# Optimization experiments

Hardware: AMD Instinct MI355X
Metric: run time of the kernel (lower is better)

The kernel has to match this reference:

```python
import jax, jax.numpy as jnp
import numpy as np

N, E, D, R, L = 30000, 200000, 768, 10, 2
EPS = 1e-5

def setup_inputs() -> dict:
    key = jax.random.key(0)
    ks = jax.random.split(key, 10)
    x = jax.random.normal(ks[0], (N, D), dtype=jnp.float32)
    edge_index = jax.random.randint(ks[1], (2, E), 0, N, dtype=jnp.int64)
    edge_type = jax.random.randint(ks[2], (E,), 0, R, dtype=jnp.int64)
    s = 0.02
    W_rel = jax.random.normal(ks[3], (L, R, D, D), dtype=jnp.float32) * s
    W_root = jax.random.normal(ks[4], (L, D, D), dtype=jnp.float32) * s
    bias = jax.random.normal(ks[5], (L, D), dtype=jnp.float32) * s
    ln_g = jnp.ones((L, D), dtype=jnp.float32)
    ln_b = jnp.zeros((L, D), dtype=jnp.float32)
    return {"x": x, "edge_index": edge_index, "edge_type": edge_type,
            "W_rel": W_rel, "W_root": W_root, "bias": bias,
            "ln_g": ln_g, "ln_b": ln_b}

def _layer_norm(h, g, b):
    mu = jnp.mean(h, axis=-1, keepdims=True)
    var = jnp.mean(jnp.square(h - mu), axis=-1, keepdims=True)
    return (h - mu) * jax.lax.rsqrt(var + EPS) * g + b

def _rgcn_conv(h, src, dst, etype, W_rel, W_root, b):
    # per-relation mean aggregation: segment id = dst * R + relation
    seg = dst * R + etype  # [E]
    msgs = h[src]  # [E, D] irregular gather
    sums = jax.ops.segment_sum(msgs, seg, num_segments=N * R)  # [N*R, D]
    cnts = jax.ops.segment_sum(jnp.ones((E,), h.dtype), seg, num_segments=N * R)
    means = sums / jnp.maximum(cnts, 1.0)[:, None]
    means = means.reshape(N, R, D)
    # linearity: mean_r(W_r x_j) == W_r mean_r(x_j)
    agg = jnp.einsum('nrd,rde->ne', means, W_rel)
    return agg + h @ W_root + b

def reference(x, edge_index, edge_type, W_rel, W_root, bias, ln_g, ln_b):
    src, dst = edge_index[0], edge_index[1]
    h = x
    for i in range(L):
        h_prev = h
        h = _rgcn_conv(h, src, dst, edge_type, W_rel[i], W_root[i], bias[i])
        h = _layer_norm(h, ln_g[i], ln_b[i])
        if i > 0:
            h = h + h_prev  # residual (skipped on first layer, per source)
        # dropout is identity in eval mode
        if i < L - 1:
            h = jax.nn.relu(h)
    return h
```

## Files before the change

### kernel.cpp

```cpp
#include <hip/hip_runtime.h>

#define N_NODES 30000
#define N_EDGES 200000
#define DIM 768
#define N_REL 10
#define N_LAYERS 2
#define LN_EPS 1e-5f
#define W_ELEMS (DIM * DIM)
#define BKS 64
#define GT_MAX 1573

typedef _Float16 f16;
typedef _Float16 f16x4 __attribute__((ext_vector_type(4)));
typedef _Float16 f16x8 __attribute__((ext_vector_type(8)));
typedef float f32x4 __attribute__((ext_vector_type(4)));

#define GLD(gaddr, laddr)                                                              \
    __builtin_amdgcn_global_load_lds((const __attribute__((address_space(1))) void*)(gaddr), \
                                     (__attribute__((address_space(3))) void*)(laddr), 16, 0, 0)

__global__ void count_kernel(const int* __restrict__ ei, const int* __restrict__ et,
                             int* __restrict__ cnt, int* __restrict__ deg,
                             int* __restrict__ posmap) {
    int e = blockIdx.x * blockDim.x + threadIdx.x;
    if (e >= N_EDGES) return;
    int src = ei[e];
    int dst = ei[N_EDGES + e];
    int r = et[e];
    atomicAdd(&cnt[dst * N_REL + r], 1);
    atomicAdd(&deg[dst], 1);
    posmap[r * N_NODES + src] = 1;
}

#define PSCAN_CHUNK 118
__global__ void posscan_kernel(int* __restrict__ posmap, int* __restrict__ mr) {
    __shared__ int part[256];
    const int r = blockIdx.x;
    int* pm = posmap + (size_t)r * N_NODES;
    const int t = threadIdx.x;
    const int c0 = t * PSCAN_CHUNK;
    int s = 0;
    for (int i = 0; i < PSCAN_CHUNK; ++i) {
        const int idx = c0 + i;
        if (idx < N_NODES && pm[idx] == 1) ++s;
    }
    part[t] = s;
    __syncthreads();
    if (t == 0) {
        int a = 0;
        for (int i = 0; i < 256; ++i) { const int v = part[i]; part[i] = a; a += v; }
        mr[r] = a;
    }
    __syncthreads();
    int a = part[t];
    for (int i = 0; i < PSCAN_CHUNK; ++i) {
        const int idx = c0 + i;
        if (idx < N_NODES && pm[idx] == 1) pm[idx] = a++;
    }
}

#define SCAN_CHUNK 118
__global__ void scan_kernel(const int* __restrict__ deg, int* __restrict__ row_start,
                            int* __restrict__ cursor) {
    __shared__ int part[256];
    __shared__ int off[257];
    const int t = threadIdx.x;
    const int c0 = t * SCAN_CHUNK;
    int s = 0;
    for (int i = 0; i < SCAN_CHUNK; ++i) {
        const int idx = c0 + i;
        if (idx < N_NODES) s += deg[idx];
    }
    part[t] = s;
    __syncthreads();
    if (t == 0) {
        int a = 0;
        for (int i = 0; i < 256; ++i) { off[i] = a; a += part[i]; }
        off[256] = a;
        row_start[N_NODES] = a;
    }
    __syncthreads();
    int a = off[t];
    for (int i = 0; i < SCAN_CHUNK; ++i) {
        const int idx = c0 + i;
        if (idx < N_NODES) {
            row_start[idx] = a;
            cursor[idx] = a;
            a += deg[idx];
        }
    }
}

__global__ void zprep_kernel(const int* __restrict__ mr, int* __restrict__ zbase,
                             int* __restrict__ tile_rel) {
    if (blockIdx.x == 0 && threadIdx.x == 0) {
        int zc = 0, tc = 0;
        for (int r = 0; r < N_REL; ++r) {
            zbase[r] = zc;
            const int nt = (mr[r] + 127) >> 7;
            for (int i = 0; i < nt; ++i) tile_rel[tc + i] = r;
            tc += nt;
            zc += nt << 7;
        }
    }
}

__global__ void fill_kernel(const int* __restrict__ ei, const int* __restrict__ et,
                            const int* __restrict__ posmap, const int* __restrict__ zbase,
                            int* __restrict__ cursor, int* __restrict__ pack,
                            int* __restrict__ srclist) {
    int e = blockIdx.x * blockDim.x + threadIdx.x;
    if (e >= N_EDGES) return;
    int src = ei[e];
    int dst = ei[N_EDGES + e];
    int r = et[e];
    const int zrow = zbase[r] + posmap[r * N_NODES + src];
    int pos = atomicAdd(&cursor[dst], 1);
    pack[pos] = (r << 24) | zrow;
    srclist[zrow] = src;
}

__global__ void convx_kernel(const float* __restrict__ in, f16* __restrict__ out) {
    int idx = blockIdx.x * blockDim.x + threadIdx.x;
    if (idx >= N_NODES * DIM / 4) return;
    const float4 v = *reinterpret_cast<const float4*>(in + (size_t)idx * 4);
    f16x4 o = {(f16)v.x, (f16)v.y, (f16)v.z, (f16)v.w};
    *reinterpret_cast<f16x4*>(out + (size_t)idx * 4) = o;
}

__global__ void convw_kernel(const float* __restrict__ Wrel, const float* __restrict__ Wroot,
                             f16* __restrict__ WT, int layer) {
    __shared__ float tile[32][33];
    const int s = blockIdx.z;
    const float* src = (s < N_REL) ? (Wrel + ((size_t)layer * N_REL + s) * W_ELEMS)
                                   : (Wroot + (size_t)layer * W_ELEMS);
    const int k0 = blockIdx.x * 32;
    const int j0 = blockIdx.y * 32;
    const int tx = threadIdx.x;
    const int ty = threadIdx.y;
#pragma unroll
    for (int i = 0; i < 4; ++i)
        tile[ty + i * 8][tx] = src[(size_t)(k0 + ty + i * 8) * DIM + j0 + tx];
    __syncthreads();
    f16* dst = WT + (size_t)s * W_ELEMS;
#pragma unroll
    for (int i = 0; i < 4; ++i)
        dst[(size_t)(j0 + ty + i * 8) * DIM + k0 + tx] = (f16)tile[tx][ty + i * 8];
}

__global__ void __launch_bounds__(256)
gemm_kernel(const f16* __restrict__ A, const f16* __restrict__ WT,
            const int* __restrict__ srclist, const int* __restrict__ tile_rel,
            f16* __restrict__ Zout, float* __restrict__ aggout) {
    __shared__ alignas(128) f16 As[2][128 * BKS];
    __shared__ alignas(128) f16 Bs[2][128 * BKS];

    const int nwg = gridDim.x;
    const int orig = blockIdx.x;
    const int qq = nwg >> 3, rr = nwg & 7, xc = orig & 7, oo = orig >> 3;
    const int wg = (xc < rr ? xc * (qq + 1) : rr * (qq + 1) + (xc - rr) * qq) + oo;
    const int gt = wg / 6, jt = wg % 6;

    int rel;
    if (tile_rel != nullptr) {
        rel = tile_rel[gt];
        if (rel < 0) return;
    } else {
        rel = N_REL;
    }

    const int t = threadIdx.x;
    const int wv = t >> 6, lane = t & 63;
    const int wr = wv >> 1, wc = wv & 1;
    const f16* B = WT + (size_t)rel * W_ELEMS + (size_t)(jt * 128) * DIM;

    const f16* gA[4];
    const f16* gB[4];
#pragma unroll
    for (int q = 0; q < 4; ++q) {
        const int chunk = q * 256 + t;
        const int row = chunk >> 3;
        const int gk = (chunk & 7) ^ (row & 7);
        int arow;
        if (tile_rel != nullptr) {
            arow = srclist[gt * 128 + row];
        } else {
            arow = gt * 128 + row;
            if (arow > N_NODES - 1) arow = N_NODES - 1;
        }
        gA[q] = A + (size_t)arow * DIM + gk * 8;
        gB[q] = B + (size_t)row * DIM + gk * 8;
    }

    f32x4 acc[4][4];
#pragma unroll
    for (int i = 0; i < 4; ++i)
#pragma unroll
        for (int j = 0; j < 4; ++j) acc[i][j] = (f32x4){0.f, 0.f, 0.f, 0.f};

    const int lr16 = lane & 15, lk = lane >> 4, l7 = lane & 7;

#pragma unroll
    for (int q = 0; q < 4; ++q) {
        GLD(gA[q], (char*)As[0] + q * 4096 + wv * 1024);
        GLD(gB[q], (char*)Bs[0] + q * 4096 + wv * 1024);
    }
    __syncthreads();

    for (int ks = 0; ks < DIM / BKS; ++ks) {
        const int cur = ks & 1;
        if (ks < DIM / BKS - 1) {
#pragma unroll
            for (int q = 0; q < 4; ++q) {
                GLD(gA[q] + (ks + 1) * BKS, (char*)As[cur ^ 1] + q * 4096 + wv * 1024);
                GLD(gB[q] + (ks + 1) * BKS, (char*)Bs[cur ^ 1] + q * 4096 + wv * 1024);
            }
        }
#pragma unroll
        for (int h = 0; h < 2; ++h) {
            f16x8 a[4], b[4];
            const int cp = (((h << 2) | lk) ^ l7) * 8;
#pragma unroll
            for (int i = 0; i < 4; ++i) {
                a[i] = *(const f16x8*)&As[cur][(wr * 64 + i * 16 + lr16) * BKS + cp];
                b[i] = *(const f16x8*)&Bs[cur][(wc * 64 + i * 16 + lr16) * BKS + cp];
            }
#pragma unroll
            for (int mi = 0; mi < 4; ++mi)
#pragma unroll
                for (int ni = 0; ni < 4; ++ni)
                    acc[mi][ni] =
                        __builtin_amdgcn_mfma_f32_16x16x32_f16(a[mi], b[ni], acc[mi][ni], 0, 0, 0);
        }
        __syncthreads();
    }

    const int lrow = lk * 4, lcol = lr16;
    const int c0 = jt * 128 + wc * 64;
    if (tile_rel != nullptr) {
#pragma unroll
        for (int mi = 0; mi < 4; ++mi)
#pragma unroll
            for (int q = 0; q < 4; ++q) {
                const int z = gt * 128 + wr * 64 + mi * 16 + lrow + q;
                f16* zp = Zout + (size_t)z * DIM + c0 + lcol;
#pragma unroll
                for (int ni = 0; ni < 4; ++ni) zp[ni * 16] = (f16)acc[mi][ni][q];
            }
    } else {
#pragma unroll
        for (int mi = 0; mi < 4; ++mi)
#pragma unroll
            for (int q = 0; q < 4; ++q) {
                const int row = gt * 128 + wr * 64 + mi * 16 + lrow + q;
                if (row >= N_NODES) continue;
                float* op = aggout + (size_t)row * DIM + c0 + lcol;
#pragma unroll
                for (int ni = 0; ni < 4; ++ni) op[ni * 16] = acc[mi][ni][q];
            }
    }
}

__global__ void __launch_bounds__(192)
gather_kernel(const f16* __restrict__ Z, const int* __restrict__ row_start,
              const int* __restrict__ pack, const int* __restrict__ cnt,
              float* __restrict__ agg) {
    const int dst = blockIdx.x;
    const int lo = row_start[dst];
    const int hi = row_start[dst + 1];
    if (lo == hi) return;
    const int t = threadIdx.x;
    float a0 = 0.f, a1 = 0.f, a2 = 0.f, a3 = 0.f;
    for (int i = lo; i < hi; ++i) {
        const int p = pack[i];
        const int r = p >> 24;
        const int zrow = p & 0xFFFFFF;
        const float inv = 1.0f / (float)cnt[dst * N_REL + r];
        const f16x4 v = *reinterpret_cast<const f16x4*>(Z + (size_t)zrow * DIM + t * 4);
        a0 += (float)v[0] * inv;
        a1 += (float)v[1] * inv;
        a2 += (float)v[2] * inv;
        a3 += (float)v[3] * inv;
    }
    float* ap = agg + (size_t)dst * DIM + t * 4;
    float4 c = *reinterpret_cast<float4*>(ap);
    c.x += a0; c.y += a1; c.z += a2; c.w += a3;
    *reinterpret_cast<float4*>(ap) = c;
}

__device__ __forceinline__ float block_reduce_sum(float v, float* sm) {
#pragma unroll
    for (int o = 32; o > 0; o >>= 1) v += __shfl_down(v, o, 64);
    const int wid = threadIdx.x >> 6;
    const int lane = threadIdx.x & 63;
    __syncthreads();
    if (lane == 0) sm[wid] = v;
    __syncthreads();
    return sm[0] + sm[1] + sm[2] + sm[3];
}

__global__ void __launch_bounds__(256)
ln_kernel(const float* __restrict__ agg, const float* __restrict__ bias,
          const float* __restrict__ g, const float* __restrict__ beta,
          const f16* __restrict__ resid16, float* __restrict__ outf32,
          f16* __restrict__ outf16, int do_relu) {
    __shared__ float sm[4];
    const int n = blockIdx.x;
    const int t = threadIdx.x;
    float v[3];
    float s = 0.f;
#pragma unroll
    for (int i = 0; i < 3; ++i) {
        const int d = t + i * 256;
        v[i] = agg[(size_t)n * DIM + d] + bias[d];
        s += v[i];
    }
    const float mu = block_reduce_sum(s, sm) * (1.0f / DIM);
    float s2 = 0.f;
#pragma unroll
    for (int i = 0; i < 3; ++i) {
        const float c = v[i] - mu;
        s2 += c * c;
    }
    const float var = block_reduce_sum(s2, sm) * (1.0f / DIM);
    const float inv = rsqrtf(var + LN_EPS);
#pragma unroll
    for (int i = 0; i < 3; ++i) {
        const int d = t + i * 256;
        float o = (v[i] - mu) * inv * g[d] + beta[d];
        if (resid16 != nullptr) o += (float)resid16[(size_t)n * DIM + d];
        if (do_relu) o = fmaxf(o, 0.f);
        if (outf32 != nullptr) outf32[(size_t)n * DIM + d] = o;
        if (outf16 != nullptr) outf16[(size_t)n * DIM + d] = (f16)o;
    }
}

extern "C" void kernel_launch(void* const* d_in, const int* in_sizes, int n_in,
                              void* d_out, int out_size, void* d_ws, size_t ws_size,
                              hipStream_t stream) {
    const float* x      = (const float*)d_in[0];
    const int*   ei     = (const int*)d_in[1];
    const int*   et     = (const int*)d_in[2];
    const float* W_rel  = (const float*)d_in[3];
    const float* W_root = (const float*)d_in[4];
    const float* bias   = (const float*)d_in[5];
    const float* ln_g   = (const float*)d_in[6];
    const float* ln_b   = (const float*)d_in[7];
    float* out = (float*)d_out;

    char* w = (char*)d_ws;
    auto alloc = [&](size_t bytes) -> char* {
        char* p = w;
        w += (bytes + 255) & ~(size_t)255;
        return p;
    };
    f16* hf16      = (f16*)alloc((size_t)N_NODES * DIM * 2);
    f16* WT        = (f16*)alloc((size_t)(N_REL + 1) * W_ELEMS * 2);
    int* cnt       = (int*)alloc((size_t)N_NODES * N_REL * 4);
    int* deg       = (int*)alloc((size_t)N_NODES * 4);
    int* row_start = (int*)alloc((size_t)(N_NODES + 1) * 4);
    int* cursor    = (int*)alloc((size_t)N_NODES * 4);
    int* pack      = (int*)alloc((size_t)N_EDGES * 4);
    int* posmap    = (int*)alloc((size_t)N_REL * N_NODES * 4);
    int* mr        = (int*)alloc(64);
    int* zbase     = (int*)alloc(64);
    int* tile_rel  = (int*)alloc((size_t)GT_MAX * 4);
    int* srclist   = (int*)alloc((size_t)GT_MAX * 128 * 4);
    f16* Zg        = (f16*)w;

    hipMemsetAsync(cnt, 0, (size_t)N_NODES * N_REL * 4, stream);
    hipMemsetAsync(deg, 0, (size_t)N_NODES * 4, stream);
    hipMemsetAsync(posmap, 0xFF, (size_t)N_REL * N_NODES * 4, stream);
    hipMemsetAsync(tile_rel, 0xFF, (size_t)GT_MAX * 4, stream);
    hipMemsetAsync(srclist, 0, (size_t)GT_MAX * 128 * 4, stream);
    count_kernel<<<(N_EDGES + 255) / 256, 256, 0, stream>>>(ei, et, cnt, deg, posmap);
    posscan_kernel<<<N_REL, 256, 0, stream>>>(posmap, mr);
    scan_kernel<<<1, 256, 0, stream>>>(deg, row_start, cursor);
    zprep_kernel<<<1, 64, 0, stream>>>(mr, zbase, tile_rel);
    fill_kernel<<<(N_EDGES + 255) / 256, 256, 0, stream>>>(ei, et, posmap, zbase, cursor,
                                                           pack, srclist);
    convx_kernel<<<(N_NODES * DIM / 4 + 255) / 256, 256, 0, stream>>>(x, hf16);

    const int mt = (N_NODES + 127) / 128;
    for (int l = 0; l < N_LAYERS; ++l) {
        convw_kernel<<<dim3(24, 24, N_REL + 1), dim3(32, 8), 0, stream>>>(W_rel, W_root, WT, l);

        gemm_kernel<<<mt * 6, 256, 0, stream>>>(hf16, WT, nullptr, nullptr,
                                                (f16*)nullptr, out);
        gemm_kernel<<<GT_MAX * 6, 256, 0, stream>>>(hf16, WT, srclist, tile_rel, Zg, nullptr);
        gather_kernel<<<N_NODES, 192, 0, stream>>>(Zg, row_start, pack, cnt, out);

        ln_kernel<<<N_NODES, 256, 0, stream>>>(
            out, bias + (size_t)l * DIM, ln_g + (size_t)l * DIM, ln_b + (size_t)l * DIM,
            (l > 0) ? hf16 : nullptr,
            (l == N_LAYERS - 1) ? out : nullptr,
            (l < N_LAYERS - 1) ? hf16 : nullptr,
            (l < N_LAYERS - 1) ? 1 : 0);
    }
}
```

Before: 1.172 ms.

## Triple-buffer GEMM LDS tiles with one barrier per k-step

Moves the GEMM's shared-memory staging from double to triple buffering and issues loads two k-steps ahead. Explicit vmcnt waits and a single barrier per iteration replace the trailing __syncthreads. The aim is to hide more global-to-LDS latency and cut one barrier per step. It raises LDS use from 64KB to 96KB per block, which may lower occupancy, and it depends on getting the hand-written waitcnt accounting right.

```diff
diff --git a/kernel.cpp b/kernel.cpp
--- a/kernel.cpp
+++ b/kernel.cpp
@@ -8,6 +8,7 @@
 #define LN_EPS 1e-5f
 #define W_ELEMS (DIM * DIM)
 #define BKS 64
+#define NT (DIM / BKS)
 #define GT_MAX 1573
 
 typedef _Float16 f16;
@@ -152,8 +153,8 @@
 gemm_kernel(const f16* __restrict__ A, const f16* __restrict__ WT,
             const int* __restrict__ srclist, const int* __restrict__ tile_rel,
             f16* __restrict__ Zout, float* __restrict__ aggout) {
-    __shared__ alignas(128) f16 As[2][128 * BKS];
-    __shared__ alignas(128) f16 Bs[2][128 * BKS];
+    __shared__ alignas(128) f16 As[3][128 * BKS];
+    __shared__ alignas(128) f16 Bs[3][128 * BKS];
 
     const int nwg = gridDim.x;
     const int orig = blockIdx.x;
@@ -192,6 +193,14 @@
         gB[q] = B + (size_t)row * DIM + gk * 8;
     }
 
+#define STAGE(buf, ks)                                                                   \
+    do {                                                                                 \
+        _Pragma("unroll") for (int q = 0; q < 4; ++q) {                                  \
+            GLD(gA[q] + (ks) * BKS, (char*)As[buf] + q * 4096 + wv * 1024);              \
+            GLD(gB[q] + (ks) * BKS, (char*)Bs[buf] + q * 4096 + wv * 1024);              \
+        }                                                                                \
+    } while (0)
+
     f32x4 acc[4][4];
 #pragma unroll
     for (int i = 0; i < 4; ++i)
@@ -200,22 +209,21 @@
 
     const int lr16 = lane & 15, lk = lane >> 4, l7 = lane & 7;
 
-#pragma unroll
-    for (int q = 0; q < 4; ++q) {
-        GLD(gA[q], (char*)As[0] + q * 4096 + wv * 1024);
-        GLD(gB[q], (char*)Bs[0] + q * 4096 + wv * 1024);
-    }
-    __syncthreads();
-
-    for (int ks = 0; ks < DIM / BKS; ++ks) {
-        const int cur = ks & 1;
-        if (ks < DIM / BKS - 1) {
-#pragma unroll
-            for (int q = 0; q < 4; ++q) {
-                GLD(gA[q] + (ks + 1) * BKS, (char*)As[cur ^ 1] + q * 4096 + wv * 1024);
-                GLD(gB[q] + (ks + 1) * BKS, (char*)Bs[cur ^ 1] + q * 4096 + wv * 1024);
-            }
+    STAGE(0, 0);
+    STAGE(1, 1);
+
+#pragma unroll
+    for (int ks = 0; ks < NT; ++ks) {
+        const int cur = ks % 3;
+        if (ks == NT - 1) {
+            asm volatile("s_waitcnt vmcnt(0)" ::: "memory");
+        } else {
+            asm volatile("s_waitcnt vmcnt(8)" ::: "memory");
         }
+        __builtin_amdgcn_sched_barrier(0);
+        __builtin_amdgcn_s_barrier();
+        if (ks + 2 < NT) STAGE((ks + 2) % 3, ks + 2);
+
 #pragma unroll
         for (int h = 0; h < 2; ++h) {
             f16x8 a[4], b[4];
@@ -232,8 +240,8 @@
                     acc[mi][ni] =
                         __builtin_amdgcn_mfma_f32_16x16x32_f16(a[mi], b[ni], acc[mi][ni], 0, 0, 0);
         }
-        __syncthreads();
-    }
+    }
+#undef STAGE
 
     const int lrow = lk * 4, lcol = lr16;
     const int c0 = jt * 128 + wc * 64;
```

Result: slower. 1.350 ms (+15.2%).

## Merge root and relation GEMMs into one launch and fuse gather with layernorm

Applied to the files above, without the earlier changes.

The root-weight GEMM tiles are appended to the relation tile list, so a single GEMM launch covers both and the tail of one overlaps the other. The gather kernel now also applies bias, layer norm, residual and ReLU, using 4-wide vector accesses. This removes one launch and one read/write pass over the fp32 aggregate buffer per layer. Out-of-place gather writes back into the same out buffer per node row, so correctness relies on each block owning its own row.

```diff
diff --git a/kernel.cpp b/kernel.cpp
--- a/kernel.cpp
+++ b/kernel.cpp
@@ -8,7 +8,10 @@
 #define LN_EPS 1e-5f
 #define W_ELEMS (DIM * DIM)
 #define BKS 64
+#define NT (DIM / BKS)
 #define GT_MAX 1573
+#define N_ROOT_TILES ((N_NODES + 127) / 128)
+#define GT_ALL (GT_MAX + N_ROOT_TILES)
 
 typedef _Float16 f16;
 typedef _Float16 f16x4 __attribute__((ext_vector_type(4)));
@@ -102,6 +105,7 @@
             tc += nt;
             zc += nt << 7;
         }
+        for (int i = 0; i < N_ROOT_TILES; ++i) tile_rel[tc + i] = N_REL + i;
     }
 }
 
@@ -161,13 +165,10 @@
     const int wg = (xc < rr ? xc * (qq + 1) : rr * (qq + 1) + (xc - rr) * qq) + oo;
     const int gt = wg / 6, jt = wg % 6;
 
-    int rel;
-    if (tile_rel != nullptr) {
-        rel = tile_rel[gt];
-        if (rel < 0) return;
-    } else {
-        rel = N_REL;
-    }
+    const int v = tile_rel[gt];
+    if (v < 0) return;
+    const bool comp = (v < N_REL);
+    const int rel = comp ? v : N_REL;
 
     const int t = threadIdx.x;
     const int wv = t >> 6, lane = t & 63;
@@ -182,10 +183,10 @@
         const int row = chunk >> 3;
         const int gk = (chunk & 7) ^ (row & 7);
         int arow;
-        if (tile_rel != nullptr) {
+        if (comp) {
             arow = srclist[gt * 128 + row];
         } else {
-            arow = gt * 128 + row;
+            arow = (v - N_REL) * 128 + row;
             if (arow > N_NODES - 1) arow = N_NODES - 1;
         }
         gA[q] = A + (size_t)arow * DIM + gk * 8;
@@ -207,9 +208,9 @@
     }
     __syncthreads();
 
-    for (int ks = 0; ks < DIM / BKS; ++ks) {
+    for (int ks = 0; ks < NT; ++ks) {
         const int cur = ks & 1;
-        if (ks < DIM / BKS - 1) {
+        if (ks < NT - 1) {
 #pragma unroll
             for (int q = 0; q < 4; ++q) {
                 GLD(gA[q] + (ks + 1) * BKS, (char*)As[cur ^ 1] + q * 4096 + wv * 1024);
@@ -237,7 +238,7 @@
 
     const int lrow = lk * 4, lcol = lr16;
     const int c0 = jt * 128 + wc * 64;
-    if (tile_rel != nullptr) {
+    if (comp) {
 #pragma unroll
         for (int mi = 0; mi < 4; ++mi)
 #pragma unroll
@@ -252,7 +253,7 @@
         for (int mi = 0; mi < 4; ++mi)
 #pragma unroll
             for (int q = 0; q < 4; ++q) {
-                const int row = gt * 128 + wr * 64 + mi * 16 + lrow + q;
+                const int row = (v - N_REL) * 128 + wr * 64 + mi * 16 + lrow + q;
                 if (row >= N_NODES) continue;
                 float* op = aggout + (size_t)row * DIM + c0 + lcol;
 #pragma unroll
@@ -261,77 +262,71 @@
     }
 }
 
+__device__ __forceinline__ float block_reduce3(float v, float* sm) {
+#pragma unroll
+    for (int o = 32; o > 0; o >>= 1) v += __shfl_down(v, o, 64);
+    const int wid = threadIdx.x >> 6;
+    const int lane = threadIdx.x & 63;
+    __syncthreads();
+    if (lane == 0) sm[wid] = v;
+    __syncthreads();
+    return sm[0] + sm[1] + sm[2];
+}
+
 __global__ void __launch_bounds__(192)
-gather_kernel(const f16* __restrict__ Z, const int* __restrict__ row_start,
-              const int* __restrict__ pack, const int* __restrict__ cnt,
-              float* __restrict__ agg) {
+gather_ln_kernel(const f16* __restrict__ Z, const int* __restrict__ row_start,
+                 const int* __restrict__ pack, const int* __restrict__ cnt,
+                 const float* __restrict__ agg, const float* __restrict__ bias,
+                 const float* __restrict__ g, const float* __restrict__ beta,
+                 const f16* __restrict__ resid16, float* __restrict__ outf32,
+                 f16* __restrict__ outf16, int do_relu) {
+    __shared__ float sm[3];
     const int dst = blockIdx.x;
+    const int t = threadIdx.x;
     const int lo = row_start[dst];
     const int hi = row_start[dst + 1];
-    if (lo == hi) return;
-    const int t = threadIdx.x;
-    float a0 = 0.f, a1 = 0.f, a2 = 0.f, a3 = 0.f;
+
+    const float4 root = *reinterpret_cast<const float4*>(agg + (size_t)dst * DIM + t * 4);
+    float a0 = root.x, a1 = root.y, a2 = root.z, a3 = root.w;
     for (int i = lo; i < hi; ++i) {
         const int p = pack[i];
         const int r = p >> 24;
         const int zrow = p & 0xFFFFFF;
         const float inv = 1.0f / (float)cnt[dst * N_REL + r];
-        const f16x4 v = *reinterpret_cast<const f16x4*>(Z + (size_t)zrow * DIM + t * 4);
-        a0 += (float)v[0] * inv;
-        a1 += (float)v[1] * inv;
-        a2 += (float)v[2] * inv;
-        a3 += (float)v[3] * inv;
-    }
-    float* ap = agg + (size_t)dst * DIM + t * 4;
-    float4 c = *reinterpret_cast<float4*>(ap);
-    c.x += a0; c.y += a1; c.z += a2; c.w += a3;
-    *reinterpret_cast<float4*>(ap) = c;
-}
-
-__device__ __forceinline__ float block_reduce_sum(float v, float* sm) {
-#pragma unroll
-    for (int o = 32; o > 0; o >>= 1) v += __shfl_down(v, o, 64);
-    const int wid = threadIdx.x >> 6;
-    const int lane = threadIdx.x & 63;
-    __syncthreads();
-    if (lane == 0) sm[wid] = v;
-    __syncthreads();
-    return sm[0] + sm[1] + sm[2] + sm[3];
-}
-
-__global__ void __launch_bounds__(256)
-ln_kernel(const float* __restrict__ agg, const float* __restrict__ bias,
-          const float* __restrict__ g, const float* __restrict__ beta,
-          const f16* __restrict__ resid16, float* __restrict__ outf32,
-          f16* __restrict__ outf16, int do_relu) {
-    __shared__ float sm[4];
-    const int n = blockIdx.x;
-    const int t = threadIdx.x;
-    float v[3];
-    float s = 0.f;
-#pragma unroll
-    for (int i = 0; i < 3; ++i) {
-        const int d = t + i * 256;
-        v[i] = agg[(size_t)n * DIM + d] + bias[d];
-        s += v[i];
-    }
-    const float mu = block_reduce_sum(s, sm) * (1.0f / DIM);
-    float s2 = 0.f;
-#pragma unroll
-    for (int i = 0; i < 3; ++i) {
-        const float c = v[i] - mu;
-        s2 += c * c;
-    }
-    const float var = block_reduce_sum(s2, sm) * (1.0f / DIM);
+        const f16x4 zv = *reinterpret_cast<const f16x4*>(Z + (size_t)zrow * DIM + t * 4);
+        a0 += (float)zv[0] * inv;
+        a1 += (float)zv[1] * inv;
+        a2 += (float)zv[2] * inv;
+        a3 += (float)zv[3] * inv;
+    }
+    const float4 b4 = *reinterpret_cast<const float4*>(bias + t * 4);
+    a0 += b4.x; a1 += b4.y; a2 += b4.z; a3 += b4.w;
+
+    const float mu = block_reduce3(a0 + a1 + a2 + a3, sm) * (1.0f / DIM);
+    const float c0 = a0 - mu, c1 = a1 - mu, c2 = a2 - mu, c3 = a3 - mu;
+    const float var = block_reduce3(c0 * c0 + c1 * c1 + c2 * c2 + c3 * c3, sm) * (1.0f / DIM);
     const float inv = rsqrtf(var + LN_EPS);
-#pragma unroll
-    for (int i = 0; i < 3; ++i) {
-        const int d = t + i * 256;
-        float o = (v[i] - mu) * inv * g[d] + beta[d];
-        if (resid16 != nullptr) o += (float)resid16[(size_t)n * DIM + d];
-        if (do_relu) o = fmaxf(o, 0.f);
-        if (outf32 != nullptr) outf32[(size_t)n * DIM + d] = o;
-        if (outf16 != nullptr) outf16[(size_t)n * DIM + d] = (f16)o;
+
+    const float4 g4 = *reinterpret_cast<const float4*>(g + t * 4);
+    const float4 be4 = *reinterpret_cast<const float4*>(beta + t * 4);
+    float o0 = c0 * inv * g4.x + be4.x;
+    float o1 = c1 * inv * g4.y + be4.y;
+    float o2 = c2 * inv * g4.z + be4.z;
+    float o3 = c3 * inv * g4.w + be4.w;
+    if (resid16 != nullptr) {
+        const f16x4 rv = *reinterpret_cast<const f16x4*>(resid16 + (size_t)dst * DIM + t * 4);
+        o0 += (float)rv[0]; o1 += (float)rv[1]; o2 += (float)rv[2]; o3 += (float)rv[3];
+    }
+    if (do_relu) {
+        o0 = fmaxf(o0, 0.f); o1 = fmaxf(o1, 0.f); o2 = fmaxf(o2, 0.f); o3 = fmaxf(o3, 0.f);
+    }
+    if (outf32 != nullptr) {
+        float4 ov = {o0, o1, o2, o3};
+        *reinterpret_cast<float4*>(outf32 + (size_t)dst * DIM + t * 4) = ov;
+    }
+    if (outf16 != nullptr) {
+        f16x4 hv = {(f16)o0, (f16)o1, (f16)o2, (f16)o3};
+        *reinterpret_cast<f16x4*>(outf16 + (size_t)dst * DIM + t * 4) = hv;
     }
 }
 
@@ -364,14 +359,14 @@
     int* posmap    = (int*)alloc((size_t)N_REL * N_NODES * 4);
     int* mr        = (int*)alloc(64);
     int* zbase     = (int*)alloc(64);
-    int* tile_rel  = (int*)alloc((size_t)GT_MAX * 4);
+    int* tile_rel  = (int*)alloc((size_t)GT_ALL * 4);
     int* srclist   = (int*)alloc((size_t)GT_MAX * 128 * 4);
     f16* Zg        = (f16*)w;
 
     hipMemsetAsync(cnt, 0, (size_t)N_NODES * N_REL * 4, stream);
     hipMemsetAsync(deg, 0, (size_t)N_NODES * 4, stream);
     hipMemsetAsync(posmap, 0xFF, (size_t)N_REL * N_NODES * 4, stream);
-    hipMemsetAsync(tile_rel, 0xFF, (size_t)GT_MAX * 4, stream);
+    hipMemsetAsync(tile_rel, 0xFF, (size_t)GT_ALL * 4, stream);
     hipMemsetAsync(srclist, 0, (size_t)GT_MAX * 128 * 4, stream);
     count_kernel<<<(N_EDGES + 255) / 256, 256, 0, stream>>>(ei, et, cnt, deg, posmap);
     posscan_kernel<<<N_REL, 256, 0, stream>>>(posmap, mr);
@@ -381,17 +376,14 @@
                                                            pack, srclist);
     convx_kernel<<<(N_NODES * DIM / 4 + 255) / 256, 256, 0, stream>>>(x, hf16);
 
-    const int mt = (N_NODES + 127) / 128;
     for (int l = 0; l < N_LAYERS; ++l) {
         convw_kernel<<<dim3(24, 24, N_REL + 1), dim3(32, 8), 0, stream>>>(W_rel, W_root, WT, l);
 
-        gemm_kernel<<<mt * 6, 256, 0, stream>>>(hf16, WT, nullptr, nullptr,
-                                                (f16*)nullptr, out);
-        gemm_kernel<<<GT_MAX * 6, 256, 0, stream>>>(hf16, WT, srclist, tile_rel, Zg, nullptr);
-        gather_kernel<<<N_NODES, 192, 0, stream>>>(Zg, row_start, pack, cnt, out);
-
-        ln_kernel<<<N_NODES, 256, 0, stream>>>(
-            out, bias + (size_t)l * DIM, ln_g + (size_t)l * DIM, ln_b + (size_t)l * DIM,
+        gemm_kernel<<<GT_ALL * 6, 256, 0, stream>>>(hf16, WT, srclist, tile_rel, Zg, out);
+
+        gather_ln_kernel<<<N_NODES, 192, 0, stream>>>(
+            Zg, row_start, pack, cnt, out,
+            bias + (size_t)l * DIM, ln_g + (size_t)l * DIM, ln_b + (size_t)l * DIM,
             (l > 0) ? hf16 : nullptr,
             (l == N_LAYERS - 1) ? out : nullptr,
             (l < N_LAYERS - 1) ? hf16 : nullptr,
```

Result: faster. 1.064 ms (-9.2%).
